# Performance work log

Hardware: AMD Instinct MI355X
Metric: run time of the kernel (lower is better)

## Reference

```python
import jax, jax.numpy as jnp
import numpy as np

FEATURE_DIM = 128
HIDDEN = 128
NCP = 25


def _bilinear_plane(plane, pts):
    """plane: (B,C,H,W); pts: (B,N,2) in [0,1], pts[...,0]->W axis, pts[...,1]->H axis.
    Bilinear sample with border clamping (grid_sample align_corners=True style).
    Returns (B,N,C)."""
    B, C, H, W = plane.shape
    x = jnp.clip(pts[..., 0], 0.0, 1.0) * (W - 1)
    y = jnp.clip(pts[..., 1], 0.0, 1.0) * (H - 1)
    x0 = jnp.clip(jnp.floor(x).astype(jnp.int32), 0, W - 2)
    y0 = jnp.clip(jnp.floor(y).astype(jnp.int32), 0, H - 2)
    wx = (x - x0)[:, :, None]
    wy = (y - y0)[:, :, None]
    flat = plane.reshape(B, C, H * W).transpose(0, 2, 1)  # (B, H*W, C)

    def g(yy, xx):
        idx = yy * W + xx  # (B,N)
        return jnp.take_along_axis(flat, idx[:, :, None], axis=1)  # (B,N,C)

    f00 = g(y0, x0)
    f01 = g(y0, x0 + 1)
    f10 = g(y0 + 1, x0)
    f11 = g(y0 + 1, x0 + 1)
    return (f00 * (1 - wx) * (1 - wy) + f01 * wx * (1 - wy)
            + f10 * (1 - wx) * wy + f11 * wx * wy)


def _sample_features(p, c_xz, c_xy, c_yz):
    """p: (B,N,3) in [0,1]; sum of bilinear samples from the three feature planes."""
    f = _bilinear_plane(c_xz, p[..., jnp.array([0, 2])])
    f = f + _bilinear_plane(c_xy, p[..., jnp.array([0, 1])])
    f = f + _bilinear_plane(c_yz, p[..., jnp.array([1, 2])])
    return f


def _rot6d_to_matrix(d6):
    """(...,6) -> (...,3,3) via Gram-Schmidt (pytorch3d rotation_6d_to_matrix)."""
    a1, a2 = d6[..., :3], d6[..., 3:]
    b1 = a1 / jnp.linalg.norm(a1, axis=-1, keepdims=True)
    a2p = a2 - jnp.sum(b1 * a2, axis=-1, keepdims=True) * b1
    b2 = a2p / jnp.linalg.norm(a2p, axis=-1, keepdims=True)
    b3 = jnp.cross(b1, b2)
    return jnp.stack([b1, b2, b3], axis=-2)


def setup_inputs():
    key = jax.random.key(0)
    ks = jax.random.split(key, 10)
    bs, ns, C, H = 16, 1024, FEATURE_DIM, 128
    pos = jax.random.uniform(ks[0], (bs, ns, 3), minval=0.2, maxval=0.8)
    ori = jax.random.normal(ks[1], (bs, ns, 6))
    query_pos = jnp.concatenate([pos, ori], axis=-1)
    c_xz = jax.random.normal(ks[2], (bs, C, H, H)) * 0.1
    c_xy = jax.random.normal(ks[3], (bs, C, H, H)) * 0.1
    c_yz = jax.random.normal(ks[4], (bs, C, H, H)) * 0.1
    # palm control-point grid exactly as in the torch module
    palm_y = np.linspace(-0.04, 0.04, 5)
    palm_z = np.linspace(0.0, 0.05, 5)
    palm_x = np.zeros(1)
    cp = np.stack(np.meshgrid(palm_x, palm_y, palm_z), axis=-1).reshape(-1, 3).astype(np.float32) / 0.3
    control_points = jnp.asarray(cp)
    s = 1.0 / np.sqrt(C)
    W_v = jax.random.normal(ks[5], (C, HIDDEN)) * s
    b_v = jnp.zeros((HIDDEN,))
    W_w = jax.random.normal(ks[6], (C, NCP)) * s
    b_w = jnp.zeros((NCP,))
    W_o = jax.random.normal(ks[7], (HIDDEN, C)) * (1.0 / np.sqrt(HIDDEN))
    b_o = jnp.zeros((C,))
    return {"query_pos": query_pos, "c_xz": c_xz, "c_xy": c_xy, "c_yz": c_yz,
            "control_points": control_points,
            "W_v": W_v, "b_v": b_v, "W_w": W_w, "b_w": b_w, "W_o": W_o, "b_o": b_o}


def reference(query_pos, c_xz, c_xy, c_yz, control_points, W_v, b_v, W_w, b_w, W_o, b_o):
    bs, ns, _ = query_pos.shape
    pos = query_pos[..., :3]   # (bs,ns,3)
    ori = query_pos[..., 3:]   # (bs,ns,6)
    # feature at the query point itself
    feature = _sample_features(pos, c_xz, c_xy, c_yz)  # (bs,ns,C)
    # rotate control points by the per-query SO(3) rotation
    R = _rot6d_to_matrix(ori)                          # (bs,ns,3,3)
    cp_rot = jnp.einsum('bnpd,gd->bngp', R, control_points)  # (bs,ns,NCP,3)
    anchor = pos[:, :, None, :] + cp_rot               # (bs,ns,NCP,3)
    # deformable gather: bilinear-sample features at the rotated control points
    sf = _sample_features(anchor.reshape(bs, ns * NCP, 3), c_xz, c_xy, c_yz)
    sf = sf.reshape(bs, ns, NCP, FEATURE_DIM)
    # per-control-point scalar weights from the query feature (to_weight)
    weights = feature @ W_w + b_w                      # (bs,ns,NCP)
    # value projection of sampled features (to_v), single head
    v = sf @ W_v + b_v                                 # (bs,ns,NCP,HIDDEN)
    out = jnp.einsum('bngh,bng->bnh', v, weights)      # weighted sum over control points
    out = out @ W_o + b_o + feature                    # to_out + residual
    return out
```

## Files before the change

### kernel.cpp

```cpp
#include <hip/hip_runtime.h>
#include <hip/hip_fp16.h>

#define CCH 128
#define NCP 25
#define HH  128
#define WW  128
#define NPIX (HH * WW)

__global__ __launch_bounds__(256) void transpose_f16_kernel(
    const float* __restrict__ s0, const float* __restrict__ s1, const float* __restrict__ s2,
    __half* __restrict__ d0, __half* __restrict__ d1, __half* __restrict__ d2)
{
    __shared__ float tile[64][65];
    const int z = blockIdx.z;
    const int b = z / 3, pl = z - 3 * b;
    const float* src = (pl == 0 ? s0 : pl == 1 ? s1 : s2) + (size_t)b * CCH * NPIX;
    __half* dst      = (pl == 0 ? d0 : pl == 1 ? d1 : d2) + (size_t)b * CCH * NPIX;
    const int n0 = blockIdx.x * 64;
    const int c0 = blockIdx.y * 64;
    const int tx = threadIdx.x;
    const int ty = threadIdx.y;

    #pragma unroll
    for (int cc = 0; cc < 64; cc += 4)
        tile[cc + ty][tx] = src[(size_t)(c0 + cc + ty) * NPIX + (n0 + tx)];
    __syncthreads();
    #pragma unroll
    for (int nn = 0; nn < 64; nn += 4)
        dst[(size_t)(n0 + nn + ty) * CCH + (c0 + tx)] = __float2half(tile[tx][nn + ty]);
}

union F4H { float4 f; __half2 h[4]; };

struct Ctx { int off; __half2 wxh, wyh; };

__device__ __forceinline__ Ctx mkctx(float u, float v) {
    float x = fminf(fmaxf(u, 0.f), 1.f) * 127.f;
    float y = fminf(fmaxf(v, 0.f), 1.f) * 127.f;
    int x0 = (int)floorf(x); x0 = x0 > 126 ? 126 : x0;
    int y0 = (int)floorf(y); y0 = y0 > 126 ? 126 : y0;
    Ctx c;
    c.wxh = __float2half2_rn(x - (float)x0);
    c.wyh = __float2half2_rn(y - (float)y0);
    c.off = (y0 * WW + x0) * 16;
    return c;
}

__device__ __forceinline__ void lerp4(const F4H* r, __half2 wx, __half2 wy, __half2 o[4]) {
    #pragma unroll
    for (int u = 0; u < 4; ++u) {
        __half2 top = __hfma2(__hsub2(r[1].h[u], r[0].h[u]), wx, r[0].h[u]);
        __half2 bot = __hfma2(__hsub2(r[3].h[u], r[2].h[u]), wx, r[2].h[u]);
        o[u] = __hfma2(__hsub2(bot, top), wy, top);
    }
}

__global__ __launch_bounds__(256, 4) void equi_qpw4_kernel(
    const float* __restrict__ qp,
    const __half* __restrict__ cxz,
    const __half* __restrict__ cxy,
    const __half* __restrict__ cyz,
    const float* __restrict__ cp,
    const float* __restrict__ Wv,
    const float* __restrict__ bv,
    const float* __restrict__ Ww,
    const float* __restrict__ bw,
    const float* __restrict__ Wo,
    const float* __restrict__ bo,
    float* __restrict__ out,
    int ns)
{
    const int nwg = gridDim.x;
    const int bid = blockIdx.x;
    const int qq = nwg >> 3, rr = nwg & 7;
    const int xcd = bid & 7, loc = bid >> 3;
    const int swz = (xcd < rr ? xcd * (qq + 1) : rr * (qq + 1) + (xcd - rr) * qq) + loc;

    const int q0   = swz * 16;
    const int t    = threadIdx.x;
    const int w    = t >> 6;
    const int lane = t & 63;
    const int qg   = lane >> 4;
    const int cg   = lane & 15;
    const int qloc = w * 4 + qg;
    const int qglob = q0 + qloc;
    const int b    = qglob / ns;

    const size_t planeStride = (size_t)CCH * NPIX;
    const float4* P0 = (const float4*)(cxz + (size_t)b * planeStride) + cg;
    const float4* P1 = (const float4*)(cxy + (size_t)b * planeStride) + cg;
    const float4* P2 = (const float4*)(cyz + (size_t)b * planeStride) + cg;

    const float* qptr = qp + (size_t)qglob * 9;
    const float px = qptr[0], py = qptr[1], pz = qptr[2];
    const float a1x = qptr[3], a1y = qptr[4], a1z = qptr[5];
    const float a2x = qptr[6], a2y = qptr[7], a2z = qptr[8];

    float n1 = rsqrtf(a1x * a1x + a1y * a1y + a1z * a1z);
    float b1x = a1x * n1, b1y = a1y * n1, b1z = a1z * n1;
    float dd = b1x * a2x + b1y * a2y + b1z * a2z;
    float u2x = a2x - dd * b1x, u2y = a2y - dd * b1y, u2z = a2z - dd * b1z;
    float n2 = rsqrtf(u2x * u2x + u2y * u2y + u2z * u2z);
    float b2x = u2x * n2, b2y = u2y * n2, b2z = u2z * n2;
    float b3x = b1y * b2z - b1z * b2y;
    float b3y = b1z * b2x - b1x * b2z;
    float b3z = b1x * b2y - b1y * b2x;

    __shared__ __align__(16) float sFeat[16][CCH];
    __shared__ __align__(16) float sWsum[16][CCH];
    __shared__ __align__(16) float sPre[16][CCH];
    __shared__ float sW[16][28];
    __shared__ float sSw[16];

    {
        Ctx c0 = mkctx(px, pz), c1 = mkctx(px, py), c2 = mkctx(py, pz);
        F4H r[12];
        r[0].f = P0[c0.off];  r[1].f = P0[c0.off + 16];  r[2].f = P0[c0.off + 2048];  r[3].f = P0[c0.off + 2064];
        r[4].f = P1[c1.off];  r[5].f = P1[c1.off + 16];  r[6].f = P1[c1.off + 2048];  r[7].f = P1[c1.off + 2064];
        r[8].f = P2[c2.off];  r[9].f = P2[c2.off + 16];  r[10].f = P2[c2.off + 2048]; r[11].f = P2[c2.off + 2064];
        __half2 s0[4], s1[4], s2[4];
        lerp4(&r[0], c0.wxh, c0.wyh, s0);
        lerp4(&r[4], c1.wxh, c1.wyh, s1);
        lerp4(&r[8], c2.wxh, c2.wyh, s2);
        float4 fa, fb;
        {
            __half2 u0 = __hadd2(__hadd2(s0[0], s1[0]), s2[0]);
            __half2 u1 = __hadd2(__hadd2(s0[1], s1[1]), s2[1]);
            __half2 u2 = __hadd2(__hadd2(s0[2], s1[2]), s2[2]);
            __half2 u3 = __hadd2(__hadd2(s0[3], s1[3]), s2[3]);
            float2 f0 = __half22float2(u0), f1 = __half22float2(u1);
            float2 f2 = __half22float2(u2), f3 = __half22float2(u3);
            fa = make_float4(f0.x, f0.y, f1.x, f1.y);
            fb = make_float4(f2.x, f2.y, f3.x, f3.y);
        }
        *(float4*)&sFeat[qloc][cg * 8]     = fa;
        *(float4*)&sFeat[qloc][cg * 8 + 4] = fb;
    }
    __syncthreads();

    #pragma unroll
    for (int rep = 0; rep < 2; ++rep) {
        int o = t + rep * 256;
        if (o < 16 * NCP) {
            int qi = o / NCP, g = o - qi * NCP;
            float acc = bw[g];
            #pragma unroll 8
            for (int c = 0; c < CCH; ++c)
                acc += sFeat[qi][c] * Ww[c * NCP + g];
            sW[qi][g] = acc;
        }
    }
    __syncthreads();
    if (t < 16) {
        float s = 0.f;
        #pragma unroll
        for (int g = 0; g < NCP; ++g) s += sW[t][g];
        sSw[t] = s;
    }

    float acc8[8] = {0.f, 0.f, 0.f, 0.f, 0.f, 0.f, 0.f, 0.f};
    for (int g = 0; g < NCP; ++g) {
        float cpx = cp[g * 3 + 0], cpy = cp[g * 3 + 1], cpz = cp[g * 3 + 2];
        float ax = px + b1x * cpx + b1y * cpy + b1z * cpz;
        float ay = py + b2x * cpx + b2y * cpy + b2z * cpz;
        float az = pz + b3x * cpx + b3y * cpy + b3z * cpz;
        Ctx c0 = mkctx(ax, az), c1 = mkctx(ax, ay), c2 = mkctx(ay, az);
        F4H r[12];
        r[0].f = P0[c0.off];  r[1].f = P0[c0.off + 16];  r[2].f = P0[c0.off + 2048];  r[3].f = P0[c0.off + 2064];
        r[4].f = P1[c1.off];  r[5].f = P1[c1.off + 16];  r[6].f = P1[c1.off + 2048];  r[7].f = P1[c1.off + 2064];
        r[8].f = P2[c2.off];  r[9].f = P2[c2.off + 16];  r[10].f = P2[c2.off + 2048]; r[11].f = P2[c2.off + 2064];
        __half2 s0[4], s1[4], s2[4];
        lerp4(&r[0], c0.wxh, c0.wyh, s0);
        lerp4(&r[4], c1.wxh, c1.wyh, s1);
        lerp4(&r[8], c2.wxh, c2.wyh, s2);
        float wg = sW[qloc][g];
        #pragma unroll
        for (int u = 0; u < 4; ++u) {
            __half2 su = __hadd2(__hadd2(s0[u], s1[u]), s2[u]);
            float2 f = __half22float2(su);
            acc8[2 * u]     += wg * f.x;
            acc8[2 * u + 1] += wg * f.y;
        }
    }
    *(float4*)&sWsum[qloc][cg * 8]     = make_float4(acc8[0], acc8[1], acc8[2], acc8[3]);
    *(float4*)&sWsum[qloc][cg * 8 + 4] = make_float4(acc8[4], acc8[5], acc8[6], acc8[7]);
    __syncthreads();

    {
        const int qi = t >> 4;
        const int hs = (t & 15) * 8;
        float4 bva = *(const float4*)&bv[hs];
        float4 bvb = *(const float4*)&bv[hs + 4];
        float sw = sSw[qi];
        float a0 = sw * bva.x, a1 = sw * bva.y, a2 = sw * bva.z, a3 = sw * bva.w;
        float a4 = sw * bvb.x, a5 = sw * bvb.y, a6 = sw * bvb.z, a7 = sw * bvb.w;
        #pragma unroll 4
        for (int c = 0; c < CCH; ++c) {
            float4 wva = *(const float4*)&Wv[c * CCH + hs];
            float4 wvb = *(const float4*)&Wv[c * CCH + hs + 4];
            float ws = sWsum[qi][c];
            a0 += ws * wva.x; a1 += ws * wva.y; a2 += ws * wva.z; a3 += ws * wva.w;
            a4 += ws * wvb.x; a5 += ws * wvb.y; a6 += ws * wvb.z; a7 += ws * wvb.w;
        }
        *(float4*)&sPre[qi][hs]     = make_float4(a0, a1, a2, a3);
        *(float4*)&sPre[qi][hs + 4] = make_float4(a4, a5, a6, a7);
    }
    __syncthreads();

    {
        const int qi = t >> 4;
        const int cs = (t & 15) * 8;
        float4 boa = *(const float4*)&bo[cs];
        float4 bob = *(const float4*)&bo[cs + 4];
        float4 fta = *(const float4*)&sFeat[qi][cs];
        float4 ftb = *(const float4*)&sFeat[qi][cs + 4];
        float a0 = boa.x + fta.x, a1 = boa.y + fta.y, a2 = boa.z + fta.z, a3 = boa.w + fta.w;
        float a4 = bob.x + ftb.x, a5 = bob.y + ftb.y, a6 = bob.z + ftb.z, a7 = bob.w + ftb.w;
        #pragma unroll 4
        for (int h = 0; h < CCH; ++h) {
            float4 woa = *(const float4*)&Wo[h * CCH + cs];
            float4 wob = *(const float4*)&Wo[h * CCH + cs + 4];
            float ph = sPre[qi][h];
            a0 += ph * woa.x; a1 += ph * woa.y; a2 += ph * woa.z; a3 += ph * woa.w;
            a4 += ph * wob.x; a5 += ph * wob.y; a6 += ph * wob.z; a7 += ph * wob.w;
        }
        float* op = out + (size_t)(q0 + qi) * CCH + cs;
        *(float4*)op       = make_float4(a0, a1, a2, a3);
        *(float4*)(op + 4) = make_float4(a4, a5, a6, a7);
    }
}

__device__ __forceinline__ float bilin_cf(const float* __restrict__ pl, int c, float u, float v) {
    float x = fminf(fmaxf(u, 0.f), 1.f) * (float)(WW - 1);
    float y = fminf(fmaxf(v, 0.f), 1.f) * (float)(HH - 1);
    int x0 = (int)floorf(x); x0 = x0 > (WW - 2) ? (WW - 2) : x0;
    int y0 = (int)floorf(y); y0 = y0 > (HH - 2) ? (HH - 2) : y0;
    float wx = x - (float)x0;
    float wy = y - (float)y0;
    const float* p = pl + ((size_t)c << 14) + (y0 << 7) + x0;
    float top = p[0] * (1.f - wx) + p[1] * wx;
    float bot = p[WW] * (1.f - wx) + p[WW + 1] * wx;
    return top * (1.f - wy) + bot * wy;
}

__global__ __launch_bounds__(128) void equi_attn_cf_kernel(
    const float* __restrict__ qp, const float* __restrict__ cxz,
    const float* __restrict__ cxy, const float* __restrict__ cyz,
    const float* __restrict__ cp, const float* __restrict__ Wv,
    const float* __restrict__ bv, const float* __restrict__ Ww,
    const float* __restrict__ bw, const float* __restrict__ Wo,
    const float* __restrict__ bo, float* __restrict__ out, int ns)
{
    const int q = blockIdx.x, b = q / ns, tid = threadIdx.x;
    const size_t planeStride = (size_t)CCH * NPIX;
    const float* pxz = cxz + (size_t)b * planeStride;
    const float* pxy = cxy + (size_t)b * planeStride;
    const float* pyz = cyz + (size_t)b * planeStride;
    const float* qptr = qp + (size_t)q * 9;
    const float px = qptr[0], py = qptr[1], pz = qptr[2];
    const float a1x = qptr[3], a1y = qptr[4], a1z = qptr[5];
    const float a2x = qptr[6], a2y = qptr[7], a2z = qptr[8];
    float n1 = rsqrtf(a1x * a1x + a1y * a1y + a1z * a1z);
    float b1x = a1x * n1, b1y = a1y * n1, b1z = a1z * n1;
    float dd = b1x * a2x + b1y * a2y + b1z * a2z;
    float u2x = a2x - dd * b1x, u2y = a2y - dd * b1y, u2z = a2z - dd * b1z;
    float n2 = rsqrtf(u2x * u2x + u2y * u2y + u2z * u2z);
    float b2x = u2x * n2, b2y = u2y * n2, b2z = u2z * n2;
    float b3x = b1y * b2z - b1z * b2y;
    float b3y = b1z * b2x - b1x * b2z;
    float b3z = b1x * b2y - b1y * b2x;
    __shared__ float sFeat[CCH]; __shared__ float sW[32];
    __shared__ float sWsum[CCH]; __shared__ float sPre[CCH];
    float feat = bilin_cf(pxz, tid, px, pz) + bilin_cf(pxy, tid, px, py) + bilin_cf(pyz, tid, py, pz);
    sFeat[tid] = feat;
    __syncthreads();
    if (tid < NCP) {
        float acc = bw[tid];
        for (int c = 0; c < CCH; ++c) acc += sFeat[c] * Ww[c * NCP + tid];
        sW[tid] = acc;
    }
    __syncthreads();
    float sw = 0.f;
    #pragma unroll
    for (int g = 0; g < NCP; ++g) sw += sW[g];
    float wacc = 0.f;
    for (int g = 0; g < NCP; ++g) {
        float cx = cp[g * 3 + 0], cy = cp[g * 3 + 1], cz = cp[g * 3 + 2];
        float ax = px + b1x * cx + b1y * cy + b1z * cz;
        float ay = py + b2x * cx + b2y * cy + b2z * cz;
        float az = pz + b3x * cx + b3y * cy + b3z * cz;
        wacc += sW[g] * (bilin_cf(pxz, tid, ax, az) + bilin_cf(pxy, tid, ax, ay) + bilin_cf(pyz, tid, ay, az));
    }
    sWsum[tid] = wacc;
    __syncthreads();
    float pre = sw * bv[tid];
    for (int c = 0; c < CCH; ++c) pre += sWsum[c] * Wv[c * CCH + tid];
    sPre[tid] = pre;
    __syncthreads();
    float o = bo[tid] + feat;
    for (int h = 0; h < CCH; ++h) o += sPre[h] * Wo[h * CCH + tid];
    out[(size_t)q * CCH + tid] = o;
}

extern "C" void kernel_launch(void* const* d_in, const int* in_sizes, int n_in,
                              void* d_out, int out_size, void* d_ws, size_t ws_size,
                              hipStream_t stream) {
    const float* qp  = (const float*)d_in[0];
    const float* cxz = (const float*)d_in[1];
    const float* cxy = (const float*)d_in[2];
    const float* cyz = (const float*)d_in[3];
    const float* cp  = (const float*)d_in[4];
    const float* Wv  = (const float*)d_in[5];
    const float* bv  = (const float*)d_in[6];
    const float* Ww  = (const float*)d_in[7];
    const float* bw  = (const float*)d_in[8];
    const float* Wo  = (const float*)d_in[9];
    const float* bo  = (const float*)d_in[10];
    float* out = (float*)d_out;

    const int bs = in_sizes[1] / (CCH * NPIX);
    const int ns = in_sizes[0] / (bs * 9);
    const int nq = bs * ns;

    const size_t planeFloats = (size_t)bs * CCH * NPIX;
    const size_t needBytes = 3 * planeFloats * sizeof(__half);

    if (ws_size >= needBytes && (nq % 16) == 0) {
        __half* t_xz = (__half*)d_ws;
        __half* t_xy = t_xz + planeFloats;
        __half* t_yz = t_xy + planeFloats;

        dim3 tgrid(NPIX / 64, CCH / 64, bs * 3);
        dim3 tblk(64, 4);
        transpose_f16_kernel<<<tgrid, tblk, 0, stream>>>(cxz, cxy, cyz, t_xz, t_xy, t_yz);

        equi_qpw4_kernel<<<nq / 16, 256, 0, stream>>>(
            qp, t_xz, t_xy, t_yz, cp, Wv, bv, Ww, bw, Wo, bo, out, ns);
    } else {
        equi_attn_cf_kernel<<<nq, 128, 0, stream>>>(
            qp, cxz, cxy, cyz, cp, Wv, bv, Ww, bw, Wo, bo, out, ns);
    }
}
```

Before: 299.1 us.

## Sort queries by batch and Morton cell before the gather kernel

Adds a counting sort over the queries. Each query's key is its batch index combined with a Morton code of a coarse 8x8x8 position cell, built with histogram, scan and scatter kernels. The main kernel then processes queries in sorted order and writes results back through the permutation. The aim is that queries sharing a workgroup and running at nearby times sample nearby plane texels, so the bilinear gathers hit cache more often. The cost is four extra small launches, a single-workgroup serial scan and an indirect output write pattern.

```diff
diff --git a/kernel.cpp b/kernel.cpp
--- a/kernel.cpp
+++ b/kernel.cpp
@@ -28,6 +28,61 @@
     #pragma unroll
     for (int nn = 0; nn < 64; nn += 4)
         dst[(size_t)(n0 + nn + ty) * CCH + (c0 + tx)] = __float2half(tile[tx][nn + ty]);
+}
+
+__device__ __forceinline__ unsigned spread3(unsigned v) {
+    return (v & 1u) | ((v & 2u) << 2) | ((v & 4u) << 4);
+}
+
+__global__ __launch_bounds__(256) void hist_kernel(
+    const float* __restrict__ qp, unsigned* __restrict__ keys,
+    unsigned* __restrict__ hist, int nq, int ns)
+{
+    int q = blockIdx.x * 256 + threadIdx.x;
+    if (q >= nq) return;
+    int b = q / ns;
+    float px = qp[(size_t)q * 9 + 0];
+    float py = qp[(size_t)q * 9 + 1];
+    float pz = qp[(size_t)q * 9 + 2];
+    int cx = (int)(fminf(fmaxf(px, 0.f), 1.f) * 8.f); cx = cx > 7 ? 7 : cx;
+    int cy = (int)(fminf(fmaxf(py, 0.f), 1.f) * 8.f); cy = cy > 7 ? 7 : cy;
+    int cz = (int)(fminf(fmaxf(pz, 0.f), 1.f) * 8.f); cz = cz > 7 ? 7 : cz;
+    unsigned m = spread3(cx) | (spread3(cy) << 1) | (spread3(cz) << 2);
+    unsigned key = (unsigned)b * 512u + m;
+    keys[q] = key;
+    atomicAdd(&hist[key], 1u);
+}
+
+__global__ __launch_bounds__(256) void scan_kernel(
+    const unsigned* __restrict__ hist, unsigned* __restrict__ offs, int nbins)
+{
+    __shared__ unsigned part[256];
+    __shared__ unsigned excl[256];
+    int tid = threadIdx.x;
+    int chunk = (nbins + 255) / 256;
+    int lo = tid * chunk, hi = lo + chunk < nbins ? lo + chunk : nbins;
+    unsigned s = 0;
+    for (int i = lo; i < hi; ++i) s += hist[i];
+    part[tid] = s;
+    __syncthreads();
+    if (tid == 0) {
+        unsigned a = 0;
+        for (int i = 0; i < 256; ++i) { excl[i] = a; a += part[i]; }
+    }
+    __syncthreads();
+    unsigned run = excl[tid];
+    for (int i = lo; i < hi; ++i) { unsigned h = hist[i]; offs[i] = run; run += h; }
+}
+
+__global__ __launch_bounds__(256) void scatter_kernel(
+    const unsigned* __restrict__ keys, unsigned* __restrict__ offs,
+    unsigned* __restrict__ sorted, int nq)
+{
+    int q = blockIdx.x * 256 + threadIdx.x;
+    if (q >= nq) return;
+    unsigned k = keys[q];
+    unsigned p = atomicAdd(&offs[k], 1u);
+    sorted[p] = (unsigned)q;
 }
 
 union F4H { float4 f; __half2 h[4]; };
@@ -67,6 +122,7 @@
     const float* __restrict__ bw,
     const float* __restrict__ Wo,
     const float* __restrict__ bo,
+    const unsigned* __restrict__ sorted,
     float* __restrict__ out,
     int ns)
 {
@@ -76,14 +132,13 @@
     const int xcd = bid & 7, loc = bid >> 3;
     const int swz = (xcd < rr ? xcd * (qq + 1) : rr * (qq + 1) + (xcd - rr) * qq) + loc;
 
-    const int q0   = swz * 16;
     const int t    = threadIdx.x;
     const int w    = t >> 6;
     const int lane = t & 63;
     const int qg   = lane >> 4;
     const int cg   = lane & 15;
     const int qloc = w * 4 + qg;
-    const int qglob = q0 + qloc;
+    const int qglob = (int)sorted[swz * 16 + qloc];
     const int b    = qglob / ns;
 
     const size_t planeStride = (size_t)CCH * NPIX;
@@ -210,6 +265,7 @@
     {
         const int qi = t >> 4;
         const int cs = (t & 15) * 8;
+        const int oq = (int)sorted[swz * 16 + qi];
         float4 boa = *(const float4*)&bo[cs];
         float4 bob = *(const float4*)&bo[cs + 4];
         float4 fta = *(const float4*)&sFeat[qi][cs];
@@ -224,7 +280,7 @@
             a0 += ph * woa.x; a1 += ph * woa.y; a2 += ph * woa.z; a3 += ph * woa.w;
             a4 += ph * wob.x; a5 += ph * wob.y; a6 += ph * wob.z; a7 += ph * wob.w;
         }
-        float* op = out + (size_t)(q0 + qi) * CCH + cs;
+        float* op = out + (size_t)oq * CCH + cs;
         *(float4*)op       = make_float4(a0, a1, a2, a3);
         *(float4*)(op + 4) = make_float4(a4, a5, a6, a7);
     }
@@ -321,21 +377,36 @@
     const int bs = in_sizes[1] / (CCH * NPIX);
     const int ns = in_sizes[0] / (bs * 9);
     const int nq = bs * ns;
+    const int nbins = bs * 512;
 
     const size_t planeFloats = (size_t)bs * CCH * NPIX;
-    const size_t needBytes = 3 * planeFloats * sizeof(__half);
+    const size_t planeBytes  = planeFloats * sizeof(__half);
+    size_t sortOff = 3 * planeBytes;
+    sortOff = (sortOff + 255) & ~(size_t)255;
+    const size_t keysOff   = sortOff;
+    const size_t sortedOff = keysOff + (size_t)nq * 4;
+    const size_t offsOff   = sortedOff + (size_t)nq * 4;
+    const size_t needBytes = offsOff + (size_t)nbins * 4;
 
     if (ws_size >= needBytes && (nq % 16) == 0) {
         __half* t_xz = (__half*)d_ws;
         __half* t_xy = t_xz + planeFloats;
         __half* t_yz = t_xy + planeFloats;
+        unsigned* keys   = (unsigned*)((char*)d_ws + keysOff);
+        unsigned* sorted = (unsigned*)((char*)d_ws + sortedOff);
+        unsigned* offs   = (unsigned*)((char*)d_ws + offsOff);
 
         dim3 tgrid(NPIX / 64, CCH / 64, bs * 3);
         dim3 tblk(64, 4);
         transpose_f16_kernel<<<tgrid, tblk, 0, stream>>>(cxz, cxy, cyz, t_xz, t_xy, t_yz);
 
+        hipMemsetAsync(offs, 0, (size_t)nbins * 4, stream);
+        hist_kernel<<<(nq + 255) / 256, 256, 0, stream>>>(qp, keys, offs, nq, ns);
+        scan_kernel<<<1, 256, 0, stream>>>(offs, offs, nbins);
+        scatter_kernel<<<(nq + 255) / 256, 256, 0, stream>>>(keys, offs, sorted, nq);
+
         equi_qpw4_kernel<<<nq / 16, 256, 0, stream>>>(
-            qp, t_xz, t_xy, t_yz, cp, Wv, bv, Ww, bw, Wo, bo, out, ns);
+            qp, t_xz, t_xy, t_yz, cp, Wv, bv, Ww, bw, Wo, bo, sorted, out, ns);
     } else {
         equi_attn_cf_kernel<<<nq, 128, 0, stream>>>(
             qp, cxz, cxy, cyz, cp, Wv, bv, Ww, bw, Wo, bo, out, ns);
```

Result: slower. 325.2 us (+8.7%).

## Split control-point loop across wave pairs, halving queries per block

Applied to the files above, without the earlier changes.

Each block now handles 8 queries instead of 16. Two waves share each query and split the 25 control points between them, 12 and 13. Their partial weighted sums go to separate shared buffers and are added in the value projection. The aim is more parallelism per query and shorter serial gather loops, with occupancy raised to 8 blocks per CU. In exchange, the weight GEMVs run over fewer queries per block, so weight reuse drops and redundant loads of Wv and Wo grow, and half the waves sit idle during the initial feature sampling.

```diff
diff --git a/kernel.cpp b/kernel.cpp
--- a/kernel.cpp
+++ b/kernel.cpp
@@ -55,7 +55,7 @@
     }
 }
 
-__global__ __launch_bounds__(256, 4) void equi_qpw4_kernel(
+__global__ __launch_bounds__(256, 8) void equi_tpw2_kernel(
     const float* __restrict__ qp,
     const __half* __restrict__ cxz,
     const __half* __restrict__ cxy,
@@ -76,13 +76,15 @@
     const int xcd = bid & 7, loc = bid >> 3;
     const int swz = (xcd < rr ? xcd * (qq + 1) : rr * (qq + 1) + (xcd - rr) * qq) + loc;
 
-    const int q0   = swz * 16;
+    const int q0   = swz * 8;
     const int t    = threadIdx.x;
     const int w    = t >> 6;
+    const int pair = w >> 1;
+    const int half = w & 1;
     const int lane = t & 63;
     const int qg   = lane >> 4;
     const int cg   = lane & 15;
-    const int qloc = w * 4 + qg;
+    const int qloc = pair * 4 + qg;
     const int qglob = q0 + qloc;
     const int b    = qglob / ns;
 
@@ -106,13 +108,14 @@
     float b3y = b1z * b2x - b1x * b2z;
     float b3z = b1x * b2y - b1y * b2x;
 
-    __shared__ __align__(16) float sFeat[16][CCH];
-    __shared__ __align__(16) float sWsum[16][CCH];
-    __shared__ __align__(16) float sPre[16][CCH];
-    __shared__ float sW[16][28];
-    __shared__ float sSw[16];
-
-    {
+    __shared__ __align__(16) float sFeat[8][CCH];
+    __shared__ __align__(16) float sA[8][CCH];
+    __shared__ __align__(16) float sB[8][CCH];
+    __shared__ __align__(16) float sPre[8][CCH];
+    __shared__ float sW[8][28];
+    __shared__ float sSw[8];
+
+    if (half == 0) {
         Ctx c0 = mkctx(px, pz), c1 = mkctx(px, py), c2 = mkctx(py, pz);
         F4H r[12];
         r[0].f = P0[c0.off];  r[1].f = P0[c0.off + 16];  r[2].f = P0[c0.off + 2048];  r[3].f = P0[c0.off + 2064];
@@ -122,36 +125,27 @@
         lerp4(&r[0], c0.wxh, c0.wyh, s0);
         lerp4(&r[4], c1.wxh, c1.wyh, s1);
         lerp4(&r[8], c2.wxh, c2.wyh, s2);
-        float4 fa, fb;
-        {
-            __half2 u0 = __hadd2(__hadd2(s0[0], s1[0]), s2[0]);
-            __half2 u1 = __hadd2(__hadd2(s0[1], s1[1]), s2[1]);
-            __half2 u2 = __hadd2(__hadd2(s0[2], s1[2]), s2[2]);
-            __half2 u3 = __hadd2(__hadd2(s0[3], s1[3]), s2[3]);
-            float2 f0 = __half22float2(u0), f1 = __half22float2(u1);
-            float2 f2 = __half22float2(u2), f3 = __half22float2(u3);
-            fa = make_float4(f0.x, f0.y, f1.x, f1.y);
-            fb = make_float4(f2.x, f2.y, f3.x, f3.y);
-        }
-        *(float4*)&sFeat[qloc][cg * 8]     = fa;
-        *(float4*)&sFeat[qloc][cg * 8 + 4] = fb;
-    }
-    __syncthreads();
-
-    #pragma unroll
-    for (int rep = 0; rep < 2; ++rep) {
-        int o = t + rep * 256;
-        if (o < 16 * NCP) {
-            int qi = o / NCP, g = o - qi * NCP;
-            float acc = bw[g];
-            #pragma unroll 8
-            for (int c = 0; c < CCH; ++c)
-                acc += sFeat[qi][c] * Ww[c * NCP + g];
-            sW[qi][g] = acc;
-        }
-    }
-    __syncthreads();
-    if (t < 16) {
+        __half2 u0 = __hadd2(__hadd2(s0[0], s1[0]), s2[0]);
+        __half2 u1 = __hadd2(__hadd2(s0[1], s1[1]), s2[1]);
+        __half2 u2 = __hadd2(__hadd2(s0[2], s1[2]), s2[2]);
+        __half2 u3 = __hadd2(__hadd2(s0[3], s1[3]), s2[3]);
+        float2 f0 = __half22float2(u0), f1 = __half22float2(u1);
+        float2 f2 = __half22float2(u2), f3 = __half22float2(u3);
+        *(float4*)&sFeat[qloc][cg * 8]     = make_float4(f0.x, f0.y, f1.x, f1.y);
+        *(float4*)&sFeat[qloc][cg * 8 + 4] = make_float4(f2.x, f2.y, f3.x, f3.y);
+    }
+    __syncthreads();
+
+    if (t < 8 * NCP) {
+        int qi = t / NCP, g = t - qi * NCP;
+        float acc = bw[g];
+        #pragma unroll 8
+        for (int c = 0; c < CCH; ++c)
+            acc += sFeat[qi][c] * Ww[c * NCP + g];
+        sW[qi][g] = acc;
+    }
+    __syncthreads();
+    if (t < 8) {
         float s = 0.f;
         #pragma unroll
         for (int g = 0; g < NCP; ++g) s += sW[t][g];
@@ -159,7 +153,9 @@
     }
 
     float acc8[8] = {0.f, 0.f, 0.f, 0.f, 0.f, 0.f, 0.f, 0.f};
-    for (int g = 0; g < NCP; ++g) {
+    const int gbeg = half ? 12 : 0;
+    const int gend = half ? 25 : 12;
+    for (int g = gbeg; g < gend; ++g) {
         float cpx = cp[g * 3 + 0], cpy = cp[g * 3 + 1], cpz = cp[g * 3 + 2];
         float ax = px + b1x * cpx + b1y * cpy + b1z * cpz;
         float ay = py + b2x * cpx + b2y * cpy + b2z * cpz;
@@ -182,51 +178,43 @@
             acc8[2 * u + 1] += wg * f.y;
         }
     }
-    *(float4*)&sWsum[qloc][cg * 8]     = make_float4(acc8[0], acc8[1], acc8[2], acc8[3]);
-    *(float4*)&sWsum[qloc][cg * 8 + 4] = make_float4(acc8[4], acc8[5], acc8[6], acc8[7]);
-    __syncthreads();
-
     {
-        const int qi = t >> 4;
-        const int hs = (t & 15) * 8;
+        float* dst = (half ? &sB[qloc][cg * 8] : &sA[qloc][cg * 8]);
+        *(float4*)dst       = make_float4(acc8[0], acc8[1], acc8[2], acc8[3]);
+        *(float4*)(dst + 4) = make_float4(acc8[4], acc8[5], acc8[6], acc8[7]);
+    }
+    __syncthreads();
+
+    {
+        const int qi = t >> 5;
+        const int hs = (t & 31) * 4;
         float4 bva = *(const float4*)&bv[hs];
-        float4 bvb = *(const float4*)&bv[hs + 4];
         float sw = sSw[qi];
         float a0 = sw * bva.x, a1 = sw * bva.y, a2 = sw * bva.z, a3 = sw * bva.w;
-        float a4 = sw * bvb.x, a5 = sw * bvb.y, a6 = sw * bvb.z, a7 = sw * bvb.w;
         #pragma unroll 4
         for (int c = 0; c < CCH; ++c) {
             float4 wva = *(const float4*)&Wv[c * CCH + hs];
-            float4 wvb = *(const float4*)&Wv[c * CCH + hs + 4];
-            float ws = sWsum[qi][c];
+            float ws = sA[qi][c] + sB[qi][c];
             a0 += ws * wva.x; a1 += ws * wva.y; a2 += ws * wva.z; a3 += ws * wva.w;
-            a4 += ws * wvb.x; a5 += ws * wvb.y; a6 += ws * wvb.z; a7 += ws * wvb.w;
         }
-        *(float4*)&sPre[qi][hs]     = make_float4(a0, a1, a2, a3);
-        *(float4*)&sPre[qi][hs + 4] = make_float4(a4, a5, a6, a7);
+        *(float4*)&sPre[qi][hs] = make_float4(a0, a1, a2, a3);
     }
     __syncthreads();
 
     {
-        const int qi = t >> 4;
-        const int cs = (t & 15) * 8;
+        const int qi = t >> 5;
+        const int cs = (t & 31) * 4;
         float4 boa = *(const float4*)&bo[cs];
-        float4 bob = *(const float4*)&bo[cs + 4];
         float4 fta = *(const float4*)&sFeat[qi][cs];
-        float4 ftb = *(const float4*)&sFeat[qi][cs + 4];
         float a0 = boa.x + fta.x, a1 = boa.y + fta.y, a2 = boa.z + fta.z, a3 = boa.w + fta.w;
-        float a4 = bob.x + ftb.x, a5 = bob.y + ftb.y, a6 = bob.z + ftb.z, a7 = bob.w + ftb.w;
         #pragma unroll 4
         for (int h = 0; h < CCH; ++h) {
             float4 woa = *(const float4*)&Wo[h * CCH + cs];
-            float4 wob = *(const float4*)&Wo[h * CCH + cs + 4];
             float ph = sPre[qi][h];
             a0 += ph * woa.x; a1 += ph * woa.y; a2 += ph * woa.z; a3 += ph * woa.w;
-            a4 += ph * wob.x; a5 += ph * wob.y; a6 += ph * wob.z; a7 += ph * wob.w;
         }
         float* op = out + (size_t)(q0 + qi) * CCH + cs;
-        *(float4*)op       = make_float4(a0, a1, a2, a3);
-        *(float4*)(op + 4) = make_float4(a4, a5, a6, a7);
+        *(float4*)op = make_float4(a0, a1, a2, a3);
     }
 }
 
@@ -325,7 +313,7 @@
     const size_t planeFloats = (size_t)bs * CCH * NPIX;
     const size_t needBytes = 3 * planeFloats * sizeof(__half);
 
-    if (ws_size >= needBytes && (nq % 16) == 0) {
+    if (ws_size >= needBytes && (nq % 8) == 0) {
         __half* t_xz = (__half*)d_ws;
         __half* t_xy = t_xz + planeFloats;
         __half* t_yz = t_xy + planeFloats;
@@ -334,7 +322,7 @@
         dim3 tblk(64, 4);
         transpose_f16_kernel<<<tgrid, tblk, 0, stream>>>(cxz, cxy, cyz, t_xz, t_xy, t_yz);
 
-        equi_qpw4_kernel<<<nq / 16, 256, 0, stream>>>(
+        equi_tpw2_kernel<<<nq / 8, 256, 0, stream>>>(
             qp, t_xz, t_xy, t_yz, cp, Wv, bv, Ww, bw, Wo, bo, out, ns);
     } else {
         equi_attn_cf_kernel<<<nq, 128, 0, stream>>>(
```

New measurement: 300.3 us. Within noise of the previous version (+0.4%).
